# Performance work log

Hardware: AMD Instinct MI355X
Metric: run time of the kernel (lower is better)

Reference implementation:

```python
import jax, jax.numpy as jnp
import numpy as np

N = 100_000            # particles
E = 3_200_000          # edges (avg degree 32)
DIM = 3
H = 1.0                # kernel_radius
SIGMA = 3.0 / 359.0 / np.pi / H**3   # 3D quintic kernel normalization
RHO_REF = 1.0
P_REF = 100.0          # rho_ref * (10*u_ref)**2 / gamma, gamma=1
P_BG = 0.0             # p_bg_factor * p_ref
ETA0 = 0.01            # base_viscosity
EPS = 1e-8


def _qpows(d, p):
    q = d / H
    return (jnp.maximum(0.0, 1.0 - q) ** p,
            jnp.maximum(0.0, 2.0 - q) ** p,
            jnp.maximum(0.0, 3.0 - q) ** p)


def kernel_w(d):
    q1, q2, q3 = _qpows(d, 5)
    return SIGMA * (q3 - 6.0 * q2 + 15.0 * q1)


def kernel_grad_w(d):
    q1, q2, q3 = _qpows(d, 4)
    return (SIGMA / H) * (-5.0 * q3 + 30.0 * q2 - 75.0 * q1)


def setup_inputs() -> dict:
    key = jax.random.key(0)
    k1, k2, k3, k4 = jax.random.split(key, 4)
    r = jax.random.uniform(k1, (N, DIM), dtype=jnp.float32)   # positions in unit box
    v = jax.random.normal(k2, (N, DIM), dtype=jnp.float32)    # velocity history (last frame)
    i_s = jax.random.randint(k3, (E,), 0, N)                  # receivers
    j_s = jax.random.randint(k4, (E,), 0, N)                  # senders
    return {"r": r, "v": v, "i_s": i_s, "j_s": j_s}


def reference(r, v, i_s, j_s):
    n = r.shape[0]
    # --- per-edge gather + kernel ---
    dr = r[i_s] - r[j_s]                       # displacement_fn, [E,3]
    d = jnp.sqrt(jnp.sum(dr * dr, axis=-1))    # [E]
    w = kernel_w(d)
    # --- density summation (scatter) ---
    mass = jnp.ones((n,), r.dtype)
    rho = mass * jax.ops.segment_sum(w, i_s, num_segments=n)
    # Tait EoS, gamma=1
    p = P_REF * (rho / RHO_REF - 1.0) + P_BG
    eta = jnp.full((n,), ETA0, r.dtype)

    # --- per-edge acceleration (gather particle fields to edges) ---
    rho_i, rho_j = rho[i_s], rho[j_s]
    p_i, p_j = p[i_s], p[j_s]
    eta_i, eta_j = eta[i_s], eta[j_s]
    u_i, u_j = v[i_s], v[j_s]                  # u == v in _transform
    v_i, v_j = u_i, u_j

    eta_ij = 2.0 * eta_i * eta_j / (eta_i + eta_j + EPS)
    p_ij = (rho_j * p_i + rho_i * p_j) / (rho_i + rho_j)
    # ((m_i/rho_i)^2 + (m_j/rho_j)^2)/m_i with m == 1
    wvol = (1.0 / rho_i) ** 2 + (1.0 / rho_j) ** 2
    c = wvol * kernel_grad_w(d) / (d + EPS)    # [E]

    # transport stress A = (outer(rho_i*u_i, v_i-u_i) + outer(rho_j*u_j, v_j-u_j))/2, [E,3,3]
    A = 0.5 * (rho_i[:, None, None] * u_i[:, :, None] * (v_i - u_i)[:, None, :]
               + rho_j[:, None, None] * u_j[:, :, None] * (v_j - u_j)[:, None, :])
    Ar = jnp.einsum('eij,ej->ei', A, dr)

    a_eq_8 = c[:, None] * (-p_ij[:, None] * dr + Ar + eta_ij[:, None] * (u_i - u_j))
    p_bg_i = jnp.zeros_like(p_i)               # _transform passes zeros
    a_eq_13 = (c * p_bg_i)[:, None] * dr

    # --- scatter-reduce to particles ---
    dudt = jax.ops.segment_sum(a_eq_8, i_s, num_segments=n)   # [N,3]
    dvdt = jax.ops.segment_sum(a_eq_13, i_s, num_segments=n)  # [N,3]

    # pack state outputs: [rho, p, dudt(3), dvdt(3)] -> [N,8]
    return jnp.concatenate([rho[:, None], p[:, None], dudt, dvdt], axis=1)
```

## Files before the change

### kernel.cpp

```cpp
#include <hip/hip_runtime.h>
#include <math.h>

#ifndef M_PI
#define M_PI 3.14159265358979323846
#endif

static constexpr float kSigma = (float)(3.0 / 359.0 / M_PI);
static constexpr float kPRef  = 100.0f;
static constexpr float kEps   = 1e-8f;
static constexpr float kEta   = (float)(2.0 * 0.01 * 0.01 / (0.01 + 0.01 + 1e-8));

#define CHUNK 4096
#define NSUB  8
#define BAT   6

typedef _Float16 hf4 __attribute__((ext_vector_type(4)));

__device__ __forceinline__ float pow5f(float t) { float t2 = t * t; return t2 * t2 * t; }
__device__ __forceinline__ float pow4f(float t) { float t2 = t * t; return t2 * t2; }

__global__ void k_pack(const float* __restrict__ r, float4* __restrict__ pos4, int n) {
    int i = blockIdx.x * blockDim.x + threadIdx.x;
    if (i >= n) return;
    pos4[i] = make_float4(r[3 * i], r[3 * i + 1], r[3 * i + 2], 0.f);
}

__global__ void k_hist(const int* __restrict__ i_s, int* __restrict__ ghist,
                       int nbA, int nbins, int E, int shift) {
    __shared__ int h[512];
    int t = threadIdx.x, blk = blockIdx.x;
    for (int b = t; b < nbins; b += 256) h[b] = 0;
    __syncthreads();
    int base = blk * CHUNK;
    int end = min(base + CHUNK, E);
    for (int kb = base; kb < end; kb += 256 * 4) {
        int iv[4];
#pragma unroll
        for (int b = 0; b < 4; b++) {
            int k = kb + b * 256 + t;
            iv[b] = (k < end) ? i_s[k] : -1;
        }
#pragma unroll
        for (int b = 0; b < 4; b++)
            if (iv[b] >= 0) atomicAdd(&h[iv[b] >> shift], 1);
    }
    __syncthreads();
    for (int b = t; b < nbins; b += 256)
        ghist[b * nbA + blk] = h[b];
}

__global__ void k_scan_block(const int* __restrict__ in, int* __restrict__ out,
                             int* __restrict__ bsum, int m) {
    __shared__ int s[256];
    int t = threadIdx.x;
    int i = blockIdx.x * 256 + t;
    int x = (i < m) ? in[i] : 0;
    s[t] = x;
    __syncthreads();
    for (int d = 1; d < 256; d <<= 1) {
        int v = (t >= d) ? s[t - d] : 0;
        __syncthreads();
        s[t] += v;
        __syncthreads();
    }
    if (i < m) out[i] = s[t] - x;
    if (t == 255) bsum[blockIdx.x] = s[255];
}

__global__ void k_scan_bsums(const int* __restrict__ bsum, int* __restrict__ bscan, int nb) {
    __shared__ int s[512];
    __shared__ int carry;
    int t = threadIdx.x;
    if (t == 0) carry = 0;
    __syncthreads();
    for (int base = 0; base < nb; base += 512) {
        int i = base + t;
        int x = (i < nb) ? bsum[i] : 0;
        s[t] = x;
        __syncthreads();
        for (int d = 1; d < 512; d <<= 1) {
            int v = (t >= d) ? s[t - d] : 0;
            __syncthreads();
            s[t] += v;
            __syncthreads();
        }
        if (i < nb) bscan[i] = s[t] - x + carry;
        __syncthreads();
        if (t == 511) carry += s[511];
        __syncthreads();
    }
}

__device__ __forceinline__ int scanned(const int* __restrict__ gscan,
                                       const int* __restrict__ bscan, int idx) {
    return gscan[idx] + bscan[idx >> 8];
}

__global__ void k_split(const int* __restrict__ i_s, const int* __restrict__ j_s,
                        const int* __restrict__ ghist, const int* __restrict__ gscan,
                        const int* __restrict__ bscan, int* __restrict__ pairs,
                        int nbA, int nbins, int E, int shift, int jbits) {
    __shared__ int lofs[512];
    __shared__ int ldelta[512];
    __shared__ int stage[CHUNK];
    __shared__ unsigned short binof[CHUNK];
    int t = threadIdx.x, blk = blockIdx.x;
    int base = blk * CHUNK;
    int end = min(base + CHUNK, E);
    int cnt = end - base;

    int h0 = (t < nbins) ? ghist[t * nbA + blk] : 0;
    int h1 = (t + 256 < nbins) ? ghist[(t + 256) * nbA + blk] : 0;
    lofs[t] = h0;
    lofs[t + 256] = h1;
    __syncthreads();
    for (int d = 1; d < 512; d <<= 1) {
        int v0 = (t >= d) ? lofs[t - d] : 0;
        int v1 = ((t + 256) >= d) ? lofs[t + 256 - d] : 0;
        __syncthreads();
        lofs[t] += v0;
        lofs[t + 256] += v1;
        __syncthreads();
    }
    int e0 = lofs[t] - h0;
    int e1 = lofs[t + 256] - h1;
    __syncthreads();
    lofs[t] = e0;
    lofs[t + 256] = e1;
    if (t < nbins) ldelta[t] = scanned(gscan, bscan, t * nbA + blk) - e0;
    if (t + 256 < nbins) ldelta[t + 256] = scanned(gscan, bscan, (t + 256) * nbA + blk) - e1;
    __syncthreads();

    int fmask = (1 << shift) - 1;
    for (int kb = base; kb < end; kb += 256 * 4) {
        int iv[4], jv[4];
#pragma unroll
        for (int b = 0; b < 4; b++) {
            int k = kb + b * 256 + t;
            iv[b] = (k < end) ? i_s[k] : -1;
            jv[b] = (k < end) ? j_s[k] : 0;
        }
#pragma unroll
        for (int b = 0; b < 4; b++) {
            if (iv[b] < 0) continue;
            int bin = iv[b] >> shift;
            int pos = atomicAdd(&lofs[bin], 1);
            stage[pos] = ((iv[b] & fmask) << jbits) | jv[b];
            binof[pos] = (unsigned short)bin;
        }
    }
    __syncthreads();
    for (int x = t; x < cnt; x += 256)
        pairs[x + ldelta[binof[x]]] = stage[x];
}

__global__ void __launch_bounds__(256, 6)
k_rho_bin(const float4* __restrict__ pos4, const int* __restrict__ pairs,
          const int* __restrict__ gscan, const int* __restrict__ bscan,
          float* __restrict__ part_rho, hf4* __restrict__ aux,
          int nbA, int n, int E, int shift, int jbits, int nbins) {
    __shared__ float srho[256];
    __shared__ float4 spos[256];
    __shared__ int sse[2];
    int bin = blockIdx.x >> 3, sub = blockIdx.x & (NSUB - 1);
    int t = threadIdx.x;
    int lo = bin << shift;
    srho[t] = 0.f;
    int ii = lo + t;
    spos[t] = (ii < n) ? pos4[ii] : make_float4(0.f, 0.f, 0.f, 0.f);
    if (t == 0) {
        sse[0] = scanned(gscan, bscan, bin * nbA);
        sse[1] = (bin + 1 < nbins) ? scanned(gscan, bscan, (bin + 1) * nbA) : E;
    }
    __syncthreads();
    int s = sse[0], len = sse[1] - sse[0];
    int k0 = s + (int)((long)len * sub / NSUB);
    int k1 = s + (int)((long)len * (sub + 1) / NSUB);
    int jm = (1 << jbits) - 1;
    int kb = k0;
    for (; kb + 256 * BAT <= k1; kb += 256 * BAT) {
        int pr[BAT];
#pragma unroll
        for (int b = 0; b < BAT; b++) pr[b] = pairs[kb + b * 256 + t];
        float4 rj[BAT];
#pragma unroll
        for (int b = 0; b < BAT; b++) rj[b] = pos4[pr[b] & jm];
#pragma unroll
        for (int b = 0; b < BAT; b++) {
            int slot = pr[b] >> jbits;
            float4 ri = spos[slot];
            float dx = ri.x - rj[b].x, dy = ri.y - rj[b].y, dz = ri.z - rj[b].z;
            float d = sqrtf(dx * dx + dy * dy + dz * dz);
            float t1 = fmaxf(1.f - d, 0.f);
            float t2 = fmaxf(2.f - d, 0.f);
            float t3 = fmaxf(3.f - d, 0.f);
            float w = kSigma * (pow5f(t3) - 6.f * pow5f(t2) + 15.f * pow5f(t1));
            atomicAdd(&srho[slot], w);
            hf4 h;
            h.x = (_Float16)dx; h.y = (_Float16)dy;
            h.z = (_Float16)dz; h.w = (_Float16)d;
            aux[kb + b * 256 + t] = h;
        }
    }
    for (int k = kb + t; k < k1; k += 256) {
        int pr = pairs[k];
        int slot = pr >> jbits;
        float4 rj = pos4[pr & jm];
        float4 ri = spos[slot];
        float dx = ri.x - rj.x, dy = ri.y - rj.y, dz = ri.z - rj.z;
        float d = sqrtf(dx * dx + dy * dy + dz * dz);
        float t1 = fmaxf(1.f - d, 0.f);
        float t2 = fmaxf(2.f - d, 0.f);
        float t3 = fmaxf(3.f - d, 0.f);
        float w = kSigma * (pow5f(t3) - 6.f * pow5f(t2) + 15.f * pow5f(t1));
        atomicAdd(&srho[slot], w);
        hf4 h;
        h.x = (_Float16)dx; h.y = (_Float16)dy;
        h.z = (_Float16)dz; h.w = (_Float16)d;
        aux[k] = h;
    }
    __syncthreads();
    if (ii < n) part_rho[(size_t)sub * n + ii] = srho[t];
}

__global__ void k_reduce_rho(const float* __restrict__ part_rho,
                             const float* __restrict__ v,
                             float4* __restrict__ vp4, float* __restrict__ out, int n) {
    int i = blockIdx.x * blockDim.x + threadIdx.x;
    if (i >= n) return;
    float rh = 0.f;
    for (int s = 0; s < NSUB; s++) rh += part_rho[(size_t)s * n + i];
    float pp = kPRef * (rh - 1.0f);
    vp4[i] = make_float4(v[3 * i], v[3 * i + 1], v[3 * i + 2], pp);
    float* o = out + (size_t)i * 8;
    o[0] = rh;
    o[1] = pp;
    o[5] = 0.f; o[6] = 0.f; o[7] = 0.f;
}

__global__ void __launch_bounds__(256, 6)
k_acc_bin(const float4* __restrict__ vp4, const int* __restrict__ pairs,
          const hf4* __restrict__ aux,
          const int* __restrict__ gscan, const int* __restrict__ bscan,
          float4* __restrict__ part_acc4, int nbA, int n, int E,
          int shift, int jbits, int nbins) {
    __shared__ float sax[256], say[256], saz[256];
    __shared__ float4 svp[256];
    __shared__ int sse[2];
    int bin = blockIdx.x >> 3, sub = blockIdx.x & (NSUB - 1);
    int t = threadIdx.x;
    int lo = bin << shift;
    sax[t] = 0.f; say[t] = 0.f; saz[t] = 0.f;
    int ii = lo + t;
    svp[t] = (ii < n) ? vp4[ii] : make_float4(0.f, 0.f, 0.f, 0.f);
    if (t == 0) {
        sse[0] = scanned(gscan, bscan, bin * nbA);
        sse[1] = (bin + 1 < nbins) ? scanned(gscan, bscan, (bin + 1) * nbA) : E;
    }
    __syncthreads();
    int s = sse[0], len = sse[1] - sse[0];
    int k0 = s + (int)((long)len * sub / NSUB);
    int k1 = s + (int)((long)len * (sub + 1) / NSUB);
    int jm = (1 << jbits) - 1;
    int kb = k0;
    for (; kb + 256 * BAT <= k1; kb += 256 * BAT) {
        int pr[BAT];
        hf4 hx[BAT];
#pragma unroll
        for (int b = 0; b < BAT; b++) {
            int k = kb + b * 256 + t;
            pr[b] = pairs[k];
            hx[b] = aux[k];
        }
        float4 vj[BAT];
#pragma unroll
        for (int b = 0; b < BAT; b++) vj[b] = vp4[pr[b] & jm];
#pragma unroll
        for (int b = 0; b < BAT; b++) {
            int slot = pr[b] >> jbits;
            float4 bi = svp[slot];
            float p_i = bi.w, p_j = vj[b].w;
            float rho_i = p_i * 0.01f + 1.0f;
            float rho_j = p_j * 0.01f + 1.0f;
            float dx = (float)hx[b].x, dy = (float)hx[b].y, dz = (float)hx[b].z;
            float d = (float)hx[b].w;
            float t1 = fmaxf(1.f - d, 0.f);
            float t2 = fmaxf(2.f - d, 0.f);
            float t3 = fmaxf(3.f - d, 0.f);
            float gw = kSigma * (-5.f * pow4f(t3) + 30.f * pow4f(t2) - 75.f * pow4f(t1));
            float inv_i = 1.0f / rho_i, inv_j = 1.0f / rho_j;
            float c = (inv_i * inv_i + inv_j * inv_j) * gw / (d + kEps);
            float p_ij = (rho_j * p_i + rho_i * p_j) / (rho_i + rho_j);
            atomicAdd(&sax[slot], c * (kEta * (bi.x - vj[b].x) - p_ij * dx));
            atomicAdd(&say[slot], c * (kEta * (bi.y - vj[b].y) - p_ij * dy));
            atomicAdd(&saz[slot], c * (kEta * (bi.z - vj[b].z) - p_ij * dz));
        }
    }
    for (int k = kb + t; k < k1; k += 256) {
        int pr = pairs[k];
        hf4 hx = aux[k];
        int slot = pr >> jbits;
        float4 vj = vp4[pr & jm];
        float4 bi = svp[slot];
        float p_i = bi.w, p_j = vj.w;
        float rho_i = p_i * 0.01f + 1.0f;
        float rho_j = p_j * 0.01f + 1.0f;
        float dx = (float)hx.x, dy = (float)hx.y, dz = (float)hx.z;
        float d = (float)hx.w;
        float t1 = fmaxf(1.f - d, 0.f);
        float t2 = fmaxf(2.f - d, 0.f);
        float t3 = fmaxf(3.f - d, 0.f);
        float gw = kSigma * (-5.f * pow4f(t3) + 30.f * pow4f(t2) - 75.f * pow4f(t1));
        float inv_i = 1.0f / rho_i, inv_j = 1.0f / rho_j;
        float c = (inv_i * inv_i + inv_j * inv_j) * gw / (d + kEps);
        float p_ij = (rho_j * p_i + rho_i * p_j) / (rho_i + rho_j);
        atomicAdd(&sax[slot], c * (kEta * (bi.x - vj.x) - p_ij * dx));
        atomicAdd(&say[slot], c * (kEta * (bi.y - vj.y) - p_ij * dy));
        atomicAdd(&saz[slot], c * (kEta * (bi.z - vj.z) - p_ij * dz));
    }
    __syncthreads();
    if (ii < n)
        part_acc4[(size_t)sub * n + ii] = make_float4(sax[t], say[t], saz[t], 0.f);
}

__global__ void k_reduce_acc(const float4* __restrict__ part_acc4,
                             float* __restrict__ out, int n) {
    int i = blockIdx.x * blockDim.x + threadIdx.x;
    if (i >= n) return;
    float ax = 0.f, ay = 0.f, az = 0.f;
    for (int s = 0; s < NSUB; s++) {
        float4 p = part_acc4[(size_t)s * n + i];
        ax += p.x; ay += p.y; az += p.z;
    }
    float* o = out + (size_t)i * 8 + 2;
    o[0] = ax; o[1] = ay; o[2] = az;
}

static inline char* wcarve(char*& ws, size_t bytes) {
    char* p = ws;
    ws += (bytes + 255) & ~(size_t)255;
    return p;
}

extern "C" void kernel_launch(void* const* d_in, const int* in_sizes, int n_in,
                              void* d_out, int out_size, void* d_ws, size_t ws_size,
                              hipStream_t stream) {
    const float* r = (const float*)d_in[0];
    const float* v = (const float*)d_in[1];
    const int* i_s = (const int*)d_in[2];
    const int* j_s = (const int*)d_in[3];
    int n = in_sizes[0] / 3;
    int E = in_sizes[2];
    float* out = (float*)d_out;

    int shift = 8;
    int nbins = ((n - 1) >> shift) + 1;
    while (nbins > 512) { shift++; nbins = ((n - 1) >> shift) + 1; }
    int jbits = 1;
    while ((1 << jbits) < n) jbits++;

    int nbA = (E + CHUNK - 1) / CHUNK;
    int m = nbins * nbA;
    int nb2 = (m + 255) / 256;

    char* ws = (char*)d_ws;
    float4* pos4     = (float4*)wcarve(ws, (size_t)n * 16);
    float4* vp4      = (float4*)wcarve(ws, (size_t)n * 16);
    int*    ghist    = (int*)wcarve(ws, (size_t)m * 4);
    int*    gscan    = (int*)wcarve(ws, (size_t)m * 4);
    int*    bsum     = (int*)wcarve(ws, (size_t)nb2 * 4);
    int*    bscan    = (int*)wcarve(ws, (size_t)nb2 * 4);
    int*    pairs    = (int*)wcarve(ws, (size_t)E * 4);
    hf4*    aux      = (hf4*)wcarve(ws, (size_t)E * 8);
    float*  part_rho = (float*)wcarve(ws, (size_t)NSUB * n * 4);
    float4* part_acc4= (float4*)wcarve(ws, (size_t)NSUB * n * 16);

    const int bs = 256;
    int gn = (n + bs - 1) / bs;

    k_pack<<<gn, bs, 0, stream>>>(r, pos4, n);
    k_hist<<<nbA, 256, 0, stream>>>(i_s, ghist, nbA, nbins, E, shift);
    k_scan_block<<<nb2, 256, 0, stream>>>(ghist, gscan, bsum, m);
    k_scan_bsums<<<1, 512, 0, stream>>>(bsum, bscan, nb2);
    k_split<<<nbA, 256, 0, stream>>>(i_s, j_s, ghist, gscan, bscan, pairs, nbA, nbins, E, shift, jbits);
    k_rho_bin<<<nbins * NSUB, 256, 0, stream>>>(pos4, pairs, gscan, bscan, part_rho, aux, nbA, n, E, shift, jbits, nbins);
    k_reduce_rho<<<gn, bs, 0, stream>>>(part_rho, v, vp4, out, n);
    k_acc_bin<<<nbins * NSUB, 256, 0, stream>>>(vp4, pairs, aux, gscan, bscan, part_acc4, nbA, n, E, shift, jbits, nbins);
    k_reduce_acc<<<gn, bs, 0, stream>>>(part_acc4, out, n);
}
```

Measured before the change: 193.1 us.

## Scatter split directly to global offsets with larger chunks; split bin launches in halves

The split kernel drops the shared-memory staging, local prefix scan and binof buffer. It now reads global scanned offsets per bin and atomically claims positions, writing pairs straight to global memory. Each block handles two histogram chunks with 512 threads. The rho and acc bin kernels are each launched twice over halves of the bins via a bin0 offset. This removes the shared scan and staging cost but trades coalesced writes for scattered global stores, and the extra launches add overhead.

```diff
diff --git a/kernel.cpp b/kernel.cpp
--- a/kernel.cpp
+++ b/kernel.cpp
@@ -10,9 +10,10 @@
 static constexpr float kEps   = 1e-8f;
 static constexpr float kEta   = (float)(2.0 * 0.01 * 0.01 / (0.01 + 0.01 + 1e-8));
 
-#define CHUNK 4096
-#define NSUB  8
-#define BAT   6
+#define CHUNKH 4096
+#define CHUNKS 8192
+#define NSUB   8
+#define BAT    6
 
 typedef _Float16 hf4 __attribute__((ext_vector_type(4)));
 
@@ -31,8 +32,8 @@
     int t = threadIdx.x, blk = blockIdx.x;
     for (int b = t; b < nbins; b += 256) h[b] = 0;
     __syncthreads();
-    int base = blk * CHUNK;
-    int end = min(base + CHUNK, E);
+    int base = blk * CHUNKH;
+    int end = min(base + CHUNKH, E);
     for (int kb = base; kb < end; kb += 256 * 4) {
         int iv[4];
 #pragma unroll
@@ -97,72 +98,43 @@
 }
 
 __global__ void k_split(const int* __restrict__ i_s, const int* __restrict__ j_s,
-                        const int* __restrict__ ghist, const int* __restrict__ gscan,
-                        const int* __restrict__ bscan, int* __restrict__ pairs,
-                        int nbA, int nbins, int E, int shift, int jbits) {
-    __shared__ int lofs[512];
-    __shared__ int ldelta[512];
-    __shared__ int stage[CHUNK];
-    __shared__ unsigned short binof[CHUNK];
+                        const int* __restrict__ gscan, const int* __restrict__ bscan,
+                        int* __restrict__ pairs, int nbAh, int nbins, int E,
+                        int shift, int jbits) {
+    __shared__ int cur[512];
     int t = threadIdx.x, blk = blockIdx.x;
-    int base = blk * CHUNK;
-    int end = min(base + CHUNK, E);
-    int cnt = end - base;
-
-    int h0 = (t < nbins) ? ghist[t * nbA + blk] : 0;
-    int h1 = (t + 256 < nbins) ? ghist[(t + 256) * nbA + blk] : 0;
-    lofs[t] = h0;
-    lofs[t + 256] = h1;
-    __syncthreads();
-    for (int d = 1; d < 512; d <<= 1) {
-        int v0 = (t >= d) ? lofs[t - d] : 0;
-        int v1 = ((t + 256) >= d) ? lofs[t + 256 - d] : 0;
-        __syncthreads();
-        lofs[t] += v0;
-        lofs[t + 256] += v1;
-        __syncthreads();
-    }
-    int e0 = lofs[t] - h0;
-    int e1 = lofs[t + 256] - h1;
-    __syncthreads();
-    lofs[t] = e0;
-    lofs[t + 256] = e1;
-    if (t < nbins) ldelta[t] = scanned(gscan, bscan, t * nbA + blk) - e0;
-    if (t + 256 < nbins) ldelta[t + 256] = scanned(gscan, bscan, (t + 256) * nbA + blk) - e1;
-    __syncthreads();
-
+    for (int b = t; b < nbins; b += 512)
+        cur[b] = scanned(gscan, bscan, b * nbAh + 2 * blk);
+    __syncthreads();
     int fmask = (1 << shift) - 1;
-    for (int kb = base; kb < end; kb += 256 * 4) {
+    int base = blk * CHUNKS;
+    int end = min(base + CHUNKS, E);
+    for (int kb = base; kb < end; kb += 512 * 4) {
         int iv[4], jv[4];
 #pragma unroll
         for (int b = 0; b < 4; b++) {
-            int k = kb + b * 256 + t;
+            int k = kb + b * 512 + t;
             iv[b] = (k < end) ? i_s[k] : -1;
             jv[b] = (k < end) ? j_s[k] : 0;
         }
 #pragma unroll
         for (int b = 0; b < 4; b++) {
             if (iv[b] < 0) continue;
-            int bin = iv[b] >> shift;
-            int pos = atomicAdd(&lofs[bin], 1);
-            stage[pos] = ((iv[b] & fmask) << jbits) | jv[b];
-            binof[pos] = (unsigned short)bin;
-        }
-    }
-    __syncthreads();
-    for (int x = t; x < cnt; x += 256)
-        pairs[x + ldelta[binof[x]]] = stage[x];
+            int pos = atomicAdd(&cur[iv[b] >> shift], 1);
+            pairs[pos] = ((iv[b] & fmask) << jbits) | jv[b];
+        }
+    }
 }
 
 __global__ void __launch_bounds__(256, 6)
 k_rho_bin(const float4* __restrict__ pos4, const int* __restrict__ pairs,
           const int* __restrict__ gscan, const int* __restrict__ bscan,
           float* __restrict__ part_rho, hf4* __restrict__ aux,
-          int nbA, int n, int E, int shift, int jbits, int nbins) {
+          int nbA, int n, int E, int shift, int jbits, int nbins, int bin0) {
     __shared__ float srho[256];
     __shared__ float4 spos[256];
     __shared__ int sse[2];
-    int bin = blockIdx.x >> 3, sub = blockIdx.x & (NSUB - 1);
+    int bin = bin0 + (blockIdx.x >> 3), sub = blockIdx.x & (NSUB - 1);
     int t = threadIdx.x;
     int lo = bin << shift;
     srho[t] = 0.f;
@@ -243,11 +215,11 @@
           const hf4* __restrict__ aux,
           const int* __restrict__ gscan, const int* __restrict__ bscan,
           float4* __restrict__ part_acc4, int nbA, int n, int E,
-          int shift, int jbits, int nbins) {
+          int shift, int jbits, int nbins, int bin0) {
     __shared__ float sax[256], say[256], saz[256];
     __shared__ float4 svp[256];
     __shared__ int sse[2];
-    int bin = blockIdx.x >> 3, sub = blockIdx.x & (NSUB - 1);
+    int bin = bin0 + (blockIdx.x >> 3), sub = blockIdx.x & (NSUB - 1);
     int t = threadIdx.x;
     int lo = bin << shift;
     sax[t] = 0.f; say[t] = 0.f; saz[t] = 0.f;
@@ -359,8 +331,9 @@
     int jbits = 1;
     while ((1 << jbits) < n) jbits++;
 
-    int nbA = (E + CHUNK - 1) / CHUNK;
-    int m = nbins * nbA;
+    int nbAh = (E + CHUNKH - 1) / CHUNKH;
+    int nbAs = (E + CHUNKS - 1) / CHUNKS;
+    int m = nbins * nbAh;
     int nb2 = (m + 255) / 256;
 
     char* ws = (char*)d_ws;
@@ -377,14 +350,17 @@
 
     const int bs = 256;
     int gn = (n + bs - 1) / bs;
+    int half = nbins / 2;
 
     k_pack<<<gn, bs, 0, stream>>>(r, pos4, n);
-    k_hist<<<nbA, 256, 0, stream>>>(i_s, ghist, nbA, nbins, E, shift);
+    k_hist<<<nbAh, 256, 0, stream>>>(i_s, ghist, nbAh, nbins, E, shift);
     k_scan_block<<<nb2, 256, 0, stream>>>(ghist, gscan, bsum, m);
     k_scan_bsums<<<1, 512, 0, stream>>>(bsum, bscan, nb2);
-    k_split<<<nbA, 256, 0, stream>>>(i_s, j_s, ghist, gscan, bscan, pairs, nbA, nbins, E, shift, jbits);
-    k_rho_bin<<<nbins * NSUB, 256, 0, stream>>>(pos4, pairs, gscan, bscan, part_rho, aux, nbA, n, E, shift, jbits, nbins);
+    k_split<<<nbAs, 512, 0, stream>>>(i_s, j_s, gscan, bscan, pairs, nbAh, nbins, E, shift, jbits);
+    k_rho_bin<<<half * NSUB, 256, 0, stream>>>(pos4, pairs, gscan, bscan, part_rho, aux, nbAh, n, E, shift, jbits, nbins, 0);
+    k_rho_bin<<<(nbins - half) * NSUB, 256, 0, stream>>>(pos4, pairs, gscan, bscan, part_rho, aux, nbAh, n, E, shift, jbits, nbins, half);
     k_reduce_rho<<<gn, bs, 0, stream>>>(part_rho, v, vp4, out, n);
-    k_acc_bin<<<nbins * NSUB, 256, 0, stream>>>(vp4, pairs, aux, gscan, bscan, part_acc4, nbA, n, E, shift, jbits, nbins);
+    k_acc_bin<<<half * NSUB, 256, 0, stream>>>(vp4, pairs, aux, gscan, bscan, part_acc4, nbAh, n, E, shift, jbits, nbins, 0);
+    k_acc_bin<<<(nbins - half) * NSUB, 256, 0, stream>>>(vp4, pairs, aux, gscan, bscan, part_acc4, nbAh, n, E, shift, jbits, nbins, half);
     k_reduce_acc<<<gn, bs, 0, stream>>>(part_acc4, out, n);
 }
```

After: 211.6 us. 1.1x slower.
